# Kernel tuning notes

Measured on AMD Instinct MI355X. Metric: run time of the kernel, lower is better.

The kernel has to match this reference:

```python
import jax, jax.numpy as jnp
import numpy as np

EPS = 1e-6
NUM_HEADS = 16

def rmsnorm(x, w):
    # x: [..., d], w: [d]
    norm = jax.lax.rsqrt(jnp.mean(x * x, axis=-1, keepdims=True) + EPS)
    return w * (x * norm)

def setup_inputs() -> dict:
    key = jax.random.key(0)
    ks = jax.random.split(key, 6)
    B, N, C = 2, 2048, 1024
    H = NUM_HEADS
    hd = C // H
    x = jax.random.normal(ks[0], (B, N, C), dtype=jnp.float32)
    scale = 1.0 / np.sqrt(C)
    qkv_w = jax.random.normal(ks[1], (C, 3 * C), dtype=jnp.float32) * scale
    qkv_b = jnp.zeros((3 * C,), dtype=jnp.float32)
    q_norm_w = jnp.ones((hd,), dtype=jnp.float32)
    k_norm_w = jnp.ones((hd,), dtype=jnp.float32)
    proj_w = jax.random.normal(ks[2], (C, C), dtype=jnp.float32) * scale
    proj_b = jnp.zeros((C,), dtype=jnp.float32)
    return {"x": x, "qkv_w": qkv_w, "qkv_b": qkv_b,
            "q_norm_w": q_norm_w, "k_norm_w": k_norm_w,
            "proj_w": proj_w, "proj_b": proj_b}

def reference(x, qkv_w, qkv_b, q_norm_w, k_norm_w, proj_w, proj_b):
    B, N, C = x.shape
    H = NUM_HEADS
    hd = C // H
    qkv = x @ qkv_w + qkv_b                       # [B,N,3C]
    qkv = qkv.reshape(B, N, 3, H, hd)
    q, k, v = qkv[:, :, 0], qkv[:, :, 1], qkv[:, :, 2]  # [B,N,H,hd]
    q = jnp.transpose(q, (0, 2, 1, 3))            # [B,H,N,hd]
    k = jnp.transpose(k, (0, 2, 1, 3))
    v = jnp.transpose(v, (0, 2, 1, 3))
    q = rmsnorm(q, q_norm_w)
    k = rmsnorm(k, k_norm_w)
    scores = jnp.einsum('bhqd,bhkd->bhqk', q, k) / jnp.sqrt(jnp.float32(hd))
    attn = jax.nn.softmax(scores, axis=-1)
    out = jnp.einsum('bhqk,bhkd->bhqd', attn, v)  # [B,H,N,hd]
    out = jnp.transpose(out, (0, 2, 1, 3)).reshape(B, N, C)
    return out @ proj_w + proj_b
```

## Files before the change

### kernel.cpp

```cpp
#include <hip/hip_runtime.h>

typedef unsigned short u16;
typedef unsigned int u32;
typedef __bf16 bf16x8 __attribute__((ext_vector_type(8)));
typedef float f32x4 __attribute__((ext_vector_type(4)));
typedef unsigned short u16x8 __attribute__((ext_vector_type(8)));
typedef unsigned short u16x4 __attribute__((ext_vector_type(4)));

__device__ __forceinline__ float bf2f(u16 u) {
    union { unsigned int i; float f; } c; c.i = ((unsigned int)u) << 16; return c.f;
}
__device__ __forceinline__ u16 f2bf(float f) {
    union { float f; unsigned int i; } c; c.f = f;
    unsigned int r = c.i + 0x7FFFu + ((c.i >> 16) & 1u);
    return (u16)(r >> 16);
}
__device__ __forceinline__ u16 f2bf_rtz(float f) {
    union { float f; unsigned int i; } c; c.f = f;
    return (u16)(c.i >> 16);
}
__device__ __forceinline__ float fast_exp2(float x) {
#if __has_builtin(__builtin_amdgcn_exp2f)
    return __builtin_amdgcn_exp2f(x);
#else
    return exp2f(x);
#endif
}
__device__ __forceinline__ bf16x8 u2b(u16x8 v) {
    return __builtin_bit_cast(bf16x8, v);
}
__device__ __forceinline__ void async16(const void* g, void* l) {
    __builtin_amdgcn_global_load_lds(
        (const __attribute__((address_space(1))) u32*)g,
        (__attribute__((address_space(3))) u32*)l, 16, 0, 0);
}

__global__ __launch_bounds__(256) void prep(
    const float* __restrict__ X, u16* __restrict__ Xb,
    const float* __restrict__ qkv_w, u16* __restrict__ qwT,
    const float* __restrict__ proj_w, u16* __restrict__ pwT)
{
    __shared__ float tile[32][33];
    const int blk = blockIdx.x;
    const int t = threadIdx.x;
    if (blk < 2048) {
        const size_t i = ((size_t)blk * 256 + t) * 8;
        u16x8 h;
        #pragma unroll
        for (int e = 0; e < 8; ++e) h[e] = f2bf(X[i + e]);
        *(u16x8*)&Xb[i] = h;
        return;
    }
    const float* W; u16* Th; int K, N, bx, by;
    if (blk < 5120) {
        W = qkv_w; Th = qwT; K = 1024; N = 3072;
        bx = (blk - 2048) % 96; by = (blk - 2048) / 96;
    } else {
        W = proj_w; Th = pwT; K = 1024; N = 1024;
        bx = (blk - 5120) % 32; by = (blk - 5120) / 32;
    }
    const int bk = by * 32, bn = bx * 32;
    const int tx = t & 31, ty = t >> 5;
    #pragma unroll
    for (int r = ty; r < 32; r += 8)
        tile[r][tx] = W[(size_t)(bk + r) * N + bn + tx];
    __syncthreads();
    if (t < 128) {
        const int row = t >> 2;
        const int c8 = (t & 3) * 8;
        u16x8 h;
        #pragma unroll
        for (int e = 0; e < 8; ++e) h[e] = f2bf(tile[c8 + e][row]);
        *(u16x8*)&Th[(size_t)(bn + row) * K + bk + c8] = h;
    }
}

__global__ __launch_bounds__(512, 2) void gemm_qkv(
    const u16* __restrict__ AH, const u16* __restrict__ BH,
    const float* __restrict__ bias,
    u16* __restrict__ Qb, u16* __restrict__ Kb, u16* __restrict__ Vt,
    const float* __restrict__ qw, const float* __restrict__ kw)
{
    const int K = 1024;
    __shared__ __align__(16) u16 AhT[2 * 256 * 32];
    __shared__ __align__(16) u16 BhT[2 * 256 * 32];
    const int t = threadIdx.x;
    const int bm = blockIdx.y * 256, bn = blockIdx.x * 256;
    const int wave = t >> 6, lane = t & 63;
    const int wm = (wave >> 2) * 128, wn = (wave & 3) * 64;
    const int l15 = lane & 15, quad = lane >> 4;
    const int srow = lane >> 2;
    const int scol = (((lane & 3) ^ ((lane >> 3) & 3))) * 8;
    const int rq = (quad ^ ((l15 >> 1) & 3)) * 8;

    f32x4 acc[8][4];
    const f32x4 zero = {0.0f, 0.0f, 0.0f, 0.0f};
    #pragma unroll
    for (int mi = 0; mi < 8; ++mi)
        #pragma unroll
        for (int nj = 0; nj < 4; ++nj) acc[mi][nj] = zero;

    #pragma unroll
    for (int ps = 0; ps < 2; ++ps)
        #pragma unroll
        for (int g = 0; g < 2; ++g) {
            const int r0 = (g * 8 + wave) * 16;
            async16(&AH[(size_t)(bm + r0 + srow) * K + ps * 32 + scol],
                    &AhT[ps * 8192 + r0 * 32]);
            async16(&BH[(size_t)(bn + r0 + srow) * K + ps * 32 + scol],
                    &BhT[ps * 8192 + r0 * 32]);
        }

    for (int ks = 0; ks < 32; ++ks) {
        if (ks == 31) asm volatile("s_waitcnt vmcnt(0)" ::: "memory");
        else          asm volatile("s_waitcnt vmcnt(4)" ::: "memory");
        __builtin_amdgcn_sched_barrier(0);
        __builtin_amdgcn_s_barrier();

        const int cb = (ks & 1) * 8192;
        bf16x8 ah[8], bh[4];
        #pragma unroll
        for (int mi = 0; mi < 8; ++mi)
            ah[mi] = *(const bf16x8*)&AhT[cb + (wm + mi * 16 + l15) * 32 + rq];
        #pragma unroll
        for (int nj = 0; nj < 4; ++nj)
            bh[nj] = *(const bf16x8*)&BhT[cb + (wn + nj * 16 + l15) * 32 + rq];
        #pragma unroll
        for (int mi = 0; mi < 8; ++mi)
            #pragma unroll
            for (int nj = 0; nj < 4; ++nj)
                acc[mi][nj] = __builtin_amdgcn_mfma_f32_16x16x32_bf16(
                    ah[mi], bh[nj], acc[mi][nj], 0, 0, 0);

        __builtin_amdgcn_sched_barrier(0);
        __builtin_amdgcn_s_barrier();
        if (ks + 2 < 32) {
            const int kk = (ks + 2) * 32;
            #pragma unroll
            for (int g = 0; g < 2; ++g) {
                const int r0 = (g * 8 + wave) * 16;
                async16(&AH[(size_t)(bm + r0 + srow) * K + kk + scol],
                        &AhT[cb + r0 * 32]);
                async16(&BH[(size_t)(bn + r0 + srow) * K + kk + scol],
                        &BhT[cb + r0 * 32]);
            }
            __builtin_amdgcn_sched_barrier(0);
        }
    }

    const int gc0 = bn + wn;
    const int sec = gc0 >> 10;
    const int h = (gc0 & 1023) >> 6;
    const int b = bm >> 11;
    const int bhd = b * 16 + h;
    float bv[4], wj[4];
    #pragma unroll
    for (int j = 0; j < 4; ++j) {
        const int d = j * 16 + l15;
        bv[j] = bias[gc0 + d];
        wj[j] = (sec == 2) ? 0.0f : (sec ? kw[d] : qw[d] * 0.18033688011f);
    }
    if (sec < 2) {
        u16* dst = sec ? Kb : Qb;
        #pragma unroll
        for (int mi = 0; mi < 8; ++mi) {
            float val[4][4];
            float ss[4] = {0.0f, 0.0f, 0.0f, 0.0f};
            #pragma unroll
            for (int j = 0; j < 4; ++j)
                #pragma unroll
                for (int r = 0; r < 4; ++r) {
                    val[j][r] = acc[mi][j][r] + bv[j];
                    ss[r] += val[j][r] * val[j][r];
                }
            #pragma unroll
            for (int r = 0; r < 4; ++r) {
                #pragma unroll
                for (int m = 1; m < 16; m <<= 1)
                    ss[r] += __shfl_xor(ss[r], m, 64);
                const float nrm = rsqrtf(ss[r] * 0.015625f + 1e-6f);
                const int n = (bm + wm + mi * 16 + quad * 4 + r) & 2047;
                const size_t rowb = ((size_t)bhd * 2048 + n) * 64;
                u16x4 pk;
                #pragma unroll
                for (int j = 0; j < 4; ++j)
                    pk[j] = f2bf(val[j][r] * nrm * wj[j]);
                *(u16x4*)&dst[rowb + l15 * 4] = pk;
            }
        }
    } else {
        #pragma unroll
        for (int mi = 0; mi < 8; ++mi) {
            const int i = mi & 3;
            const int nb = (bm + wm + (mi >> 2) * 64) & 2047;
            const int s0 = (i & 1) * 32 + quad * 8 + (i >> 1) * 4;
            #pragma unroll
            for (int j = 0; j < 4; ++j) {
                const int d = j * 16 + l15;
                u16x4 pk;
                #pragma unroll
                for (int r = 0; r < 4; ++r)
                    pk[r] = f2bf(acc[mi][j][r] + bv[j]);
                *(u16x4*)&Vt[((size_t)bhd * 64 + d) * 2048 + nb + s0] = pk;
            }
        }
    }
}

__global__ __launch_bounds__(256) void gemm_proj(
    const u16* __restrict__ AH, const u16* __restrict__ BH,
    const float* __restrict__ bias, float* __restrict__ C)
{
    const int N = 1024, K = 1024;
    __shared__ __align__(16) u16 AhT[4 * 64 * 32];
    __shared__ __align__(16) u16 BhT[4 * 128 * 32];
    const int t = threadIdx.x;
    const int bm = blockIdx.y * 64, bn = blockIdx.x * 128;
    const int wave = t >> 6, lane = t & 63;
    const int l15 = lane & 15, quad = lane >> 4;
    const int srow = lane >> 2;
    const int scol = (((lane & 3) ^ ((lane >> 3) & 3))) * 8;
    const int rq = (quad ^ ((l15 >> 1) & 3)) * 8;

    f32x4 acc[4][2];
    const f32x4 zero = {0.0f, 0.0f, 0.0f, 0.0f};
    #pragma unroll
    for (int i = 0; i < 4; ++i)
        #pragma unroll
        for (int j = 0; j < 2; ++j) acc[i][j] = zero;

    for (int k0 = 0; k0 < K; k0 += 128) {
        #pragma unroll
        for (int s = 0; s < 4; ++s) {
            const int kk = k0 + s * 32;
            {
                const int r0 = wave * 16;
                async16(&AH[(size_t)(bm + r0 + srow) * K + kk + scol],
                        &AhT[s * 2048 + r0 * 32]);
            }
            #pragma unroll
            for (int cc = 0; cc < 2; ++cc) {
                const int r0 = (wave * 2 + cc) * 16;
                async16(&BH[(size_t)(bn + r0 + srow) * K + kk + scol],
                        &BhT[s * 4096 + r0 * 32]);
            }
        }
        __syncthreads();
        #pragma unroll
        for (int s = 0; s < 4; ++s) {
            const int ab = s * 2048, bb = s * 4096;
            bf16x8 ah[4], bh[2];
            #pragma unroll
            for (int i = 0; i < 4; ++i)
                ah[i] = *(const bf16x8*)&AhT[ab + (i * 16 + l15) * 32 + rq];
            #pragma unroll
            for (int j = 0; j < 2; ++j)
                bh[j] = *(const bf16x8*)
                    &BhT[bb + (wave * 32 + j * 16 + l15) * 32 + rq];
            #pragma unroll
            for (int i = 0; i < 4; ++i)
                #pragma unroll
                for (int j = 0; j < 2; ++j)
                    acc[i][j] = __builtin_amdgcn_mfma_f32_16x16x32_bf16(
                        ah[i], bh[j], acc[i][j], 0, 0, 0);
        }
        __syncthreads();
    }

    #pragma unroll
    for (int j = 0; j < 2; ++j) {
        const int col = bn + wave * 32 + j * 16 + l15;
        const float bv = bias[col];
        #pragma unroll
        for (int i = 0; i < 4; ++i) {
            const int row = bm + i * 16 + quad * 4;
            #pragma unroll
            for (int r = 0; r < 4; ++r)
                C[(size_t)(row + r) * N + col] = acc[i][j][r] + bv;
        }
    }
}

__global__ __launch_bounds__(512) void flash_attn_mfma(
    const u16* __restrict__ Qb, const u16* __restrict__ Kb,
    const u16* __restrict__ Vt, u16* __restrict__ Attn)
{
    __shared__ __align__(16) u16 Klds[2 * 64 * 64];
    __shared__ __align__(16) u16 Vlds[2 * 64 * 64];

    const int t = threadIdx.x;
    const int bid = blockIdx.x;
    const int bh = bid & 31;
    const int qt = bid >> 5;
    const int n0 = qt * 256;
    const size_t kbase = (size_t)bh * 2048 * 64;
    const size_t vbase = (size_t)bh * 64 * 2048;
    const int wave = t >> 6, lane = t & 63;
    const int l15 = lane & 15, quad = lane >> 4;
    const int srow8 = lane >> 3;
    const int sgrp = lane & 7;

    bf16x8 qf[2][2];
    #pragma unroll
    for (int qs = 0; qs < 2; ++qs) {
        const size_t qrow =
            ((size_t)bh * 2048 + n0 + wave * 32 + qs * 16 + l15) * 64;
        qf[qs][0] = *(const bf16x8*)&Qb[qrow + quad * 8];
        qf[qs][1] = *(const bf16x8*)&Qb[qrow + 32 + quad * 8];
    }

    int kofs[4][2];
    #pragma unroll
    for (int nt = 0; nt < 4; ++nt) {
        const int row = nt * 16 + l15;
        kofs[nt][0] = row * 64 + ((quad ^ (row & 7)) * 8);
        kofs[nt][1] = row * 64 + (((quad + 4) ^ (row & 7)) * 8);
    }

    f32x4 o[2][4];
    const f32x4 zero = {0.0f, 0.0f, 0.0f, 0.0f};
    #pragma unroll
    for (int qs = 0; qs < 2; ++qs)
        #pragma unroll
        for (int dt = 0; dt < 4; ++dt) o[qs][dt] = zero;
    f32x4 osum[2] = {zero, zero};
    bf16x8 ones;
    #pragma unroll
    for (int e = 0; e < 8; ++e) ones[e] = (__bf16)1.0f;

    {
        const int r0 = wave * 8;
        const int row = r0 + srow8;
        const int gg = sgrp ^ (row & 7);
        async16(&Kb[kbase + (size_t)row * 64 + gg * 8], &Klds[r0 * 64]);
        async16(&Vt[vbase + (size_t)row * 2048 + gg * 8], &Vlds[r0 * 64]);
    }

    for (int kt = 0; kt < 32; ++kt) {
        __syncthreads();
        if (kt + 1 < 32) {
            const int nb = ((kt + 1) & 1) * 4096;
            const int r0 = wave * 8;
            const int row = r0 + srow8;
            const int gg = sgrp ^ (row & 7);
            async16(&Kb[kbase + (size_t)((kt + 1) * 64 + row) * 64 + gg * 8],
                    &Klds[nb + r0 * 64]);
            async16(&Vt[vbase + (size_t)row * 2048 + (kt + 1) * 64 + gg * 8],
                    &Vlds[nb + r0 * 64]);
        }
        const int cb = (kt & 1) * 4096;

        f32x4 s[2][4];
        #pragma unroll
        for (int nt = 0; nt < 4; ++nt) {
            bf16x8 kf0 = *(const bf16x8*)&Klds[cb + kofs[nt][0]];
            bf16x8 kf1 = *(const bf16x8*)&Klds[cb + kofs[nt][1]];
            #pragma unroll
            for (int qs = 0; qs < 2; ++qs) {
                s[qs][nt] = __builtin_amdgcn_mfma_f32_16x16x32_bf16(
                    kf0, qf[qs][0], zero, 0, 0, 0);
                s[qs][nt] = __builtin_amdgcn_mfma_f32_16x16x32_bf16(
                    kf1, qf[qs][1], s[qs][nt], 0, 0, 0);
            }
        }

        bf16x8 pf[2][2];
        #pragma unroll
        for (int qs = 0; qs < 2; ++qs) {
            #pragma unroll
            for (int m = 0; m < 2; ++m) {
                u16x8 pk;
                #pragma unroll
                for (int r = 0; r < 4; ++r) {
                    pk[r]     = f2bf_rtz(fast_exp2(s[qs][m][r]));
                    pk[4 + r] = f2bf_rtz(fast_exp2(s[qs][m + 2][r]));
                }
                pf[qs][m] = u2b(pk);
            }
        }

        #pragma unroll
        for (int dt = 0; dt < 4; ++dt) {
            bf16x8 vf0 = *(const bf16x8*)&Vlds[cb + kofs[dt][0]];
            bf16x8 vf1 = *(const bf16x8*)&Vlds[cb + kofs[dt][1]];
            #pragma unroll
            for (int qs = 0; qs < 2; ++qs) {
                o[qs][dt] = __builtin_amdgcn_mfma_f32_16x16x32_bf16(
                    pf[qs][0], vf0, o[qs][dt], 0, 0, 0);
                o[qs][dt] = __builtin_amdgcn_mfma_f32_16x16x32_bf16(
                    pf[qs][1], vf1, o[qs][dt], 0, 0, 0);
            }
        }
        #pragma unroll
        for (int qs = 0; qs < 2; ++qs) {
            osum[qs] = __builtin_amdgcn_mfma_f32_16x16x32_bf16(
                pf[qs][0], ones, osum[qs], 0, 0, 0);
            osum[qs] = __builtin_amdgcn_mfma_f32_16x16x32_bf16(
                pf[qs][1], ones, osum[qs], 0, 0, 0);
        }
    }

    const size_t obase =
        ((size_t)(bh >> 4) * 2048 + n0) * 1024 + (bh & 15) * 64;
    #pragma unroll
    for (int qs = 0; qs < 2; ++qs)
        #pragma unroll
        for (int r = 0; r < 4; ++r) {
            const float inv = 1.0f / osum[qs][r];
            const size_t rbase =
                obase + (size_t)(wave * 32 + qs * 16 + quad * 4 + r) * 1024;
            #pragma unroll
            for (int dt = 0; dt < 4; ++dt)
                Attn[rbase + dt * 16 + l15] = f2bf(o[qs][dt][r] * inv);
        }
}

extern "C" void kernel_launch(void* const* d_in, const int* in_sizes, int n_in,
                              void* d_out, int out_size, void* d_ws, size_t ws_size,
                              hipStream_t stream)
{
    const float* x      = (const float*)d_in[0];
    const float* qkv_w  = (const float*)d_in[1];
    const float* qkv_b  = (const float*)d_in[2];
    const float* q_nw   = (const float*)d_in[3];
    const float* k_nw   = (const float*)d_in[4];
    const float* proj_w = (const float*)d_in[5];
    const float* proj_b = (const float*)d_in[6];
    float* out = (float*)d_out;

    char* ws = (char*)d_ws;
    u16* AttnB = (u16*)ws;
    u16* qwT   = (u16*)(ws + 8388608);
    u16* pwT   = (u16*)(ws + 14680064);
    u16* Xb    = (u16*)(ws + 16777216);
    u16* QbB   = (u16*)(ws + 25165824);
    u16* KbB   = (u16*)(ws + 33554432);
    u16* VtB   = (u16*)(ws + 41943040);
    (void)in_sizes; (void)n_in; (void)out_size;
    if (ws_size < 50331648u) return;

    prep<<<dim3(6144), 256, 0, stream>>>(x, Xb, qkv_w, qwT, proj_w, pwT);
    gemm_qkv<<<dim3(3072 / 256, 4096 / 256), 512, 0, stream>>>(
        Xb, qwT, qkv_b, QbB, KbB, VtB, q_nw, k_nw);
    flash_attn_mfma<<<dim3(256), 512, 0, stream>>>(QbB, KbB, VtB, AttnB);
    gemm_proj<<<dim3(1024 / 128, 4096 / 64), 256, 0, stream>>>(
        AttnB, pwT, proj_b, out);
}
```

Measured before the change: 193.9 us.

## Triple-buffer LDS tiles in QKV GEMM and flash attention to drop a barrier

Grows the shared-memory staging buffers from two to three stages in both the QKV GEMM and the flash-attention kernel. Loads are now issued right after the single per-iteration barrier, which removes the second barrier in the GEMM loop and deepens the attention prefetch to two tiles with explicit vmcnt waits. This aims to cut synchronisation stalls and hide global-load latency. The cost is more LDS per block, which may lower occupancy: the GEMM's two-blocks-per-CU launch bound now needs 96KB per block.

```diff
diff --git a/kernel.cpp b/kernel.cpp
--- a/kernel.cpp
+++ b/kernel.cpp
@@ -82,8 +82,8 @@
     const float* __restrict__ qw, const float* __restrict__ kw)
 {
     const int K = 1024;
-    __shared__ __align__(16) u16 AhT[2 * 256 * 32];
-    __shared__ __align__(16) u16 BhT[2 * 256 * 32];
+    __shared__ __align__(16) u16 AhT[3 * 256 * 32];
+    __shared__ __align__(16) u16 BhT[3 * 256 * 32];
     const int t = threadIdx.x;
     const int bm = blockIdx.y * 256, bn = blockIdx.x * 256;
     const int wave = t >> 6, lane = t & 63;
@@ -116,8 +116,23 @@
         else          asm volatile("s_waitcnt vmcnt(4)" ::: "memory");
         __builtin_amdgcn_sched_barrier(0);
         __builtin_amdgcn_s_barrier();
-
-        const int cb = (ks & 1) * 8192;
+        __builtin_amdgcn_sched_barrier(0);
+
+        if (ks + 2 < 32) {
+            const int sb = ((ks + 2) % 3) * 8192;
+            const int kk = (ks + 2) * 32;
+            #pragma unroll
+            for (int g = 0; g < 2; ++g) {
+                const int r0 = (g * 8 + wave) * 16;
+                async16(&AH[(size_t)(bm + r0 + srow) * K + kk + scol],
+                        &AhT[sb + r0 * 32]);
+                async16(&BH[(size_t)(bn + r0 + srow) * K + kk + scol],
+                        &BhT[sb + r0 * 32]);
+            }
+            __builtin_amdgcn_sched_barrier(0);
+        }
+
+        const int cb = (ks % 3) * 8192;
         bf16x8 ah[8], bh[4];
         #pragma unroll
         for (int mi = 0; mi < 8; ++mi)
@@ -131,21 +146,6 @@
             for (int nj = 0; nj < 4; ++nj)
                 acc[mi][nj] = __builtin_amdgcn_mfma_f32_16x16x32_bf16(
                     ah[mi], bh[nj], acc[mi][nj], 0, 0, 0);
-
-        __builtin_amdgcn_sched_barrier(0);
-        __builtin_amdgcn_s_barrier();
-        if (ks + 2 < 32) {
-            const int kk = (ks + 2) * 32;
-            #pragma unroll
-            for (int g = 0; g < 2; ++g) {
-                const int r0 = (g * 8 + wave) * 16;
-                async16(&AH[(size_t)(bm + r0 + srow) * K + kk + scol],
-                        &AhT[cb + r0 * 32]);
-                async16(&BH[(size_t)(bn + r0 + srow) * K + kk + scol],
-                        &BhT[cb + r0 * 32]);
-            }
-            __builtin_amdgcn_sched_barrier(0);
-        }
     }
 
     const int gc0 = bn + wn;
@@ -285,8 +285,8 @@
     const u16* __restrict__ Qb, const u16* __restrict__ Kb,
     const u16* __restrict__ Vt, u16* __restrict__ Attn)
 {
-    __shared__ __align__(16) u16 Klds[2 * 64 * 64];
-    __shared__ __align__(16) u16 Vlds[2 * 64 * 64];
+    __shared__ __align__(16) u16 Klds[3 * 64 * 64];
+    __shared__ __align__(16) u16 Vlds[3 * 64 * 64];
 
     const int t = threadIdx.x;
     const int bid = blockIdx.x;
@@ -328,27 +328,36 @@
     #pragma unroll
     for (int e = 0; e < 8; ++e) ones[e] = (__bf16)1.0f;
 
-    {
+    #pragma unroll
+    for (int ps = 0; ps < 2; ++ps) {
         const int r0 = wave * 8;
         const int row = r0 + srow8;
         const int gg = sgrp ^ (row & 7);
-        async16(&Kb[kbase + (size_t)row * 64 + gg * 8], &Klds[r0 * 64]);
-        async16(&Vt[vbase + (size_t)row * 2048 + gg * 8], &Vlds[r0 * 64]);
+        async16(&Kb[kbase + (size_t)(ps * 64 + row) * 64 + gg * 8],
+                &Klds[ps * 4096 + r0 * 64]);
+        async16(&Vt[vbase + (size_t)row * 2048 + ps * 64 + gg * 8],
+                &Vlds[ps * 4096 + r0 * 64]);
     }
 
     for (int kt = 0; kt < 32; ++kt) {
-        __syncthreads();
-        if (kt + 1 < 32) {
-            const int nb = ((kt + 1) & 1) * 4096;
+        if (kt == 31) asm volatile("s_waitcnt vmcnt(0)" ::: "memory");
+        else          asm volatile("s_waitcnt vmcnt(2)" ::: "memory");
+        __builtin_amdgcn_sched_barrier(0);
+        __builtin_amdgcn_s_barrier();
+        __builtin_amdgcn_sched_barrier(0);
+
+        if (kt + 2 < 32) {
+            const int sb = ((kt + 2) % 3) * 4096;
             const int r0 = wave * 8;
             const int row = r0 + srow8;
             const int gg = sgrp ^ (row & 7);
-            async16(&Kb[kbase + (size_t)((kt + 1) * 64 + row) * 64 + gg * 8],
-                    &Klds[nb + r0 * 64]);
-            async16(&Vt[vbase + (size_t)row * 2048 + (kt + 1) * 64 + gg * 8],
-                    &Vlds[nb + r0 * 64]);
-        }
-        const int cb = (kt & 1) * 4096;
+            async16(&Kb[kbase + (size_t)((kt + 2) * 64 + row) * 64 + gg * 8],
+                    &Klds[sb + r0 * 64]);
+            async16(&Vt[vbase + (size_t)row * 2048 + (kt + 2) * 64 + gg * 8],
+                    &Vlds[sb + r0 * 64]);
+            __builtin_amdgcn_sched_barrier(0);
+        }
+        const int cb = (kt % 3) * 4096;
 
         f32x4 s[2][4];
         #pragma unroll
```

Result: no change. 192.4 us (-0.8%).
